# Performance work log

Hardware: AMD Instinct MI355X
Metric: run time of the kernel (lower is better)

## Reference

```python
import jax, jax.numpy as jnp
import numpy as np

# FlowNetC correlation hyperparameters (init_kwargs)
PAD = 4            # pad_size
KERNEL = 1         # kernel_size (1x1 patch)
MD = 4             # max_displacement
STRIDE1 = 1        # stride over output positions
STRIDE2 = 1        # stride over displacements


def setup_inputs() -> dict:
    key = jax.random.key(0)
    k1, k2 = jax.random.split(key)
    input1 = jax.random.normal(k1, (8, 256, 96, 128), dtype=jnp.float32)
    input2 = jax.random.normal(k2, (8, 256, 96, 128), dtype=jnp.float32)
    return {"input1": input1, "input2": input2}


def reference(input1, input2):
    # Cost volume: out[b, d, y, x] = (1/C) * sum_c input1[b,c,y,x] * input2[b,c,y+dy,x+dx]
    # for all displacements (dy, dx) in [-MD, MD] with step STRIDE2.
    # With pad_size == max_displacement, kernel_size == 1, stride1 == 1 the output
    # spatial grid equals the input grid (FlowNetC configuration). Normalization
    # matches correlation_cuda: sumelems = kernel_size^2 * C.
    B, C, H, W = input1.shape
    p2 = jnp.pad(input2, ((0, 0), (0, 0), (PAD, PAD), (PAD, PAD)))
    disp = range(-MD, MD + 1, STRIDE2)  # 9 offsets -> 81 displacement channels
    outs = []
    for dy in disp:
        for dx in disp:
            shifted = jax.lax.dynamic_slice(p2, (0, 0, PAD + dy, PAD + dx), (B, C, H, W))
            # mean over channels == sum / (KERNEL*KERNEL*C) since KERNEL == 1
            outs.append(jnp.mean(input1 * shifted, axis=1))
    return jnp.stack(outs, axis=1)  # [B, 81, H, W]
```

## Files before the change

### kernel.cpp

```cpp
#include <hip/hip_runtime.h>
#include <hip/hip_bf16.h>


#define B_ 8
#define C_ 256
#define H_ 96
#define W_ 128
#define HW_ 12288
#define CHW_ 3145728

#define BUFSZ 40960
#define IN1_OFF 0
#define IN2_OFF 8192
#define IN2_ROWB (32 * 64)

typedef __attribute__((ext_vector_type(8))) short short8;
typedef __attribute__((ext_vector_type(4))) float f32x4;

__device__ __forceinline__ int swz16(int g, int slot) {
    return (g ^ (slot & 3) ^ ((slot >> 2) & 3)) * 16;
}

__global__ __launch_bounds__(512, 2) void corr_mfma5(
    const float* __restrict__ in1,
    const float* __restrict__ in2,
    float* __restrict__ out)
{
    __shared__ __align__(16) char lds[2 * BUFSZ];

    const int tid = threadIdx.x;

    const int blk  = blockIdx.x;
    const int b    = blk & 7;
    const int rest = blk >> 3;
    const int yt   = rest >> 3;
    const int xh   = rest & 7;

    #pragma unroll
    for (int k = 0; k < 10; ++k)
        *(f32x4*)(lds + tid * 16 + k * 8192) = f32x4{0.f, 0.f, 0.f, 0.f};

    const int lane = tid & 63;
    const int wv   = tid >> 6;
    const int ut   = wv & 1;
    const int yrh  = wv >> 1;
    const int ln   = lane & 15;
    const int qd   = lane >> 4;

    const int offA0 = IN1_OFF + ((2 * yrh) * 16 + ln) * 64 + swz16(qd, ln);
    const int pB    = 16 * ut + ln;
    const int offB  = IN2_OFF + ((2 * yrh) * 32 + pB) * 64 + swz16(qd, pB);

    const float* in1b = in1 + (size_t)b * CHW_;
    const float* in2b = in2 + (size_t)b * CHW_;

    const int pp2 = tid & 7;
    const int g2  = (tid >> 3) & 3;
    const int r2i = tid >> 5;
    const int px2 = 4 * pp2;
    const int gx2 = xh * 16 - 8 + px2;
    const int ry2 = yt * 8 - 4 + r2i;
    const bool valid2 = (gx2 >= 0) && (gx2 <= 124) && (ry2 >= 0) && (ry2 < H_);
    const int slot2 = r2i * 32 + px2;
    const float* sp2base = in2b + (size_t)(8 * g2) * HW_ + ry2 * W_ + gx2;

    const int pq1 = tid & 3;
    const int jj1 = (tid >> 2) & 3;
    const int g1  = (tid >> 4) & 3;
    const int r1i = tid >> 6;
    const int px1 = 4 * pq1;
    const int gx1 = xh * 16 + px1;
    const int y1  = yt * 8 + r1i;
    const int slot1 = r1i * 16 + px1;
    const float* sp1base = in1b + (size_t)(8 * g1 + 2 * jj1) * HW_ + y1 * W_ + gx1;

    f32x4 r2[8], r1v[2];

    auto issue = [&](int kc) {
        const size_t ch = (size_t)kc * 32 * HW_;
        if (valid2) {
            #pragma unroll
            for (int j = 0; j < 8; ++j)
                r2[j] = *(const f32x4*)(sp2base + ch + (size_t)j * HW_);
        }
        r1v[0] = *(const f32x4*)(sp1base + ch);
        r1v[1] = *(const f32x4*)(sp1base + ch + HW_);
    };

    auto store = [&](char* __restrict__ buf) {
        if (valid2) {
            #pragma unroll
            for (int p = 0; p < 4; ++p) {
                union { __hip_bfloat162 h2[4]; short8 s8; } u;
                #pragma unroll
                for (int jj = 0; jj < 4; ++jj)
                    u.h2[jj] = __float22bfloat162_rn(float2{r2[2 * jj][p], r2[2 * jj + 1][p]});
                *(short8*)(buf + IN2_OFF + (slot2 + p) * 64 + swz16(g2, slot2 + p)) = u.s8;
            }
        }
        #pragma unroll
        for (int p = 0; p < 4; ++p) {
            __hip_bfloat162 h = __float22bfloat162_rn(float2{r1v[0][p], r1v[1][p]});
            *(__hip_bfloat162*)(buf + IN1_OFF + (slot1 + p) * 64 + swz16(g1, slot1 + p) + 4 * jj1) = h;
        }
    };

    f32x4 acc0[9], acc1[9];
    #pragma unroll
    for (int s = 0; s < 9; ++s) { acc0[s] = f32x4{0.f,0.f,0.f,0.f}; acc1[s] = f32x4{0.f,0.f,0.f,0.f}; }

    __syncthreads();

    issue(0);

    for (int kc = 0; kc < 8; ++kc) {
        char* buf = lds + (kc & 1) * BUFSZ;
        store(buf);
        if (kc < 7) issue(kc + 1);
        asm volatile("s_waitcnt lgkmcnt(0)" ::: "memory");
        __builtin_amdgcn_s_barrier();
        asm volatile("" ::: "memory");
        short8 a0  = *(const short8*)(buf + offA0);
        short8 a1  = *(const short8*)(buf + offA0 + 16 * 64);
        short8 blo = *(const short8*)(buf + offB);
        #pragma unroll
        for (int s = 0; s < 9; ++s) {
            short8 bhi = *(const short8*)(buf + offB + (s + 1) * IN2_ROWB);
            acc0[s] = __builtin_amdgcn_mfma_f32_16x16x32_bf16(a0, blo, acc0[s], 0, 0, 0);
            acc1[s] = __builtin_amdgcn_mfma_f32_16x16x32_bf16(a1, bhi, acc1[s], 0, 0, 0);
            blo = bhi;
        }
    }

    __syncthreads();

    const float scale = 1.0f / 256.0f;
    float* outb = out + (size_t)b * 81 * HW_ + (size_t)(yt * 8) * W_ + xh * 16;

    #pragma unroll
    for (int s = 0; s < 9; ++s) {
        #pragma unroll
        for (int yr = 0; yr < 2; ++yr) {
            const f32x4 a = yr ? acc1[s] : acc0[s];
            const int y = 2 * yrh + yr;
            #pragma unroll
            for (int r = 0; r < 4; ++r) {
                const int m  = qd * 4 + r;
                const int dx = ln - m - 8 + 16 * ut;
                if (dx >= -4 && dx <= 4)
                    *(float*)(lds + ((y * 9 + dx + 4) * 16 + m) * 4) = a[r] * scale;
            }
        }
        asm volatile("s_waitcnt lgkmcnt(0)" ::: "memory");
        __builtin_amdgcn_s_barrier();
        asm volatile("" ::: "memory");
        #pragma unroll
        for (int i = 0; i < 3; ++i) {
            const int pidx = i * 4 + qd;
            if (pidx < 9) {
                const float v = *(const float*)(lds + ((wv * 9 + pidx) * 16 + ln) * 4);
                outb[((size_t)(s * 9 + pidx) * H_ + wv) * W_ + ln] = v;
            }
        }
        asm volatile("s_waitcnt lgkmcnt(0)" ::: "memory");
        __builtin_amdgcn_s_barrier();
        asm volatile("" ::: "memory");
    }
}

extern "C" void kernel_launch(void* const* d_in, const int* in_sizes, int n_in,
                              void* d_out, int out_size, void* d_ws, size_t ws_size,
                              hipStream_t stream) {
    const float* in1 = (const float*)d_in[0];
    const float* in2 = (const float*)d_in[1];
    float* out = (float*)d_out;

    corr_mfma5<<<768, 512, 0, stream>>>(in1, in2, out);
}
```

Before: 247.5 us.

## Pre-convert inputs to swizzled channel-last bf16 workspace and stream via direct LDS loads

Adds a prep kernel that converts both fp32 NCHW inputs into a bf16 channel-blocked, pre-swizzled layout in the workspace. The main kernel then fills LDS with global_load_lds DMA in a two-stage prefetch, with no register staging, conversion or LDS zeroing, and out-of-bounds halo reads point at a zeroed pad. The aim is to cut per-block fp32 reload and conversion overhead for the halo-duplicated input2 tiles and to overlap loads with MFMA. The cost is an extra kernel launch plus a full write and re-read of a bf16 copy of both inputs. A fallback path keeps the old kernel when the workspace is too small.

```diff
diff --git a/kernel.cpp b/kernel.cpp
--- a/kernel.cpp
+++ b/kernel.cpp
@@ -14,6 +14,10 @@
 #define IN2_OFF 8192
 #define IN2_ROWB (32 * 64)
 
+#define PLANEB 786432
+#define IMGWS  50331648
+#define WS_NEED (2ull * IMGWS + 1024ull)
+
 typedef __attribute__((ext_vector_type(8))) short short8;
 typedef __attribute__((ext_vector_type(4))) float f32x4;
 
@@ -21,24 +25,74 @@
     return (g ^ (slot & 3) ^ ((slot >> 2) & 3)) * 16;
 }
 
-__global__ __launch_bounds__(512, 2) void corr_mfma5(
+__device__ __forceinline__ void gload16(const void* g, void* l) {
+    __builtin_amdgcn_global_load_lds(
+        (const __attribute__((address_space(1))) unsigned int*)g,
+        (__attribute__((address_space(3))) unsigned int*)l, 16, 0, 0);
+}
+
+__global__ __launch_bounds__(256) void prep(
     const float* __restrict__ in1,
     const float* __restrict__ in2,
+    char* __restrict__ ws)
+{
+    const int blk = blockIdx.x;
+    const int tid = threadIdx.x;
+
+    if (blk == 0)
+        *(float*)(ws + 2 * (size_t)IMGWS + tid * 4) = 0.f;
+
+    const int img  = (blk >= 768) ? 1 : 0;
+    const int r    = blk - img * 768;
+    const int b    = r & 7;
+    const int rest = r >> 3;
+    const int kc   = rest & 7;
+    const int yo   = rest >> 3;
+
+    const float* src = (img ? in2 : in1) + (size_t)b * CHW_ + (size_t)(kc * 32) * HW_;
+    char* dplane = ws + (size_t)img * IMGWS + (size_t)(b * 8 + kc) * PLANEB;
+
+    const int g  = tid & 3;
+    const int xq = (tid >> 2) & 15;
+    const int yl = tid >> 6;
+
+    #pragma unroll
+    for (int yi = 0; yi < 2; ++yi) {
+        const int y = yo * 8 + yi * 4 + yl;
+        #pragma unroll
+        for (int x2 = 0; x2 < 2; ++x2) {
+            const int px0 = x2 * 64 + xq * 4;
+            f32x4 v[8];
+            #pragma unroll
+            for (int jj = 0; jj < 8; ++jj)
+                v[jj] = *(const f32x4*)(src + (size_t)(8 * g + jj) * HW_ + y * W_ + px0);
+            #pragma unroll
+            for (int j = 0; j < 4; ++j) {
+                const int px = px0 + j;
+                union { __hip_bfloat162 h2[4]; short8 s8; } u;
+                #pragma unroll
+                for (int p = 0; p < 4; ++p)
+                    u.h2[p] = __float22bfloat162_rn(float2{v[2 * p][j], v[2 * p + 1][j]});
+                const int F = img ? ((px & 3) ^ (((px + 8) >> 2) & 3))
+                                  : ((px & 3) ^ ((px >> 2) & 3));
+                *(short8*)(dplane + ((size_t)y * W_ + px) * 64 + (g ^ F) * 16) = u.s8;
+            }
+        }
+    }
+}
+
+__global__ __launch_bounds__(512, 4) void corr_mfma7(
+    const char* __restrict__ ws,
     float* __restrict__ out)
 {
     __shared__ __align__(16) char lds[2 * BUFSZ];
 
     const int tid = threadIdx.x;
-
-    const int blk  = blockIdx.x;
+    const int blk = blockIdx.x;
     const int b    = blk & 7;
     const int rest = blk >> 3;
     const int yt   = rest >> 3;
     const int xh   = rest & 7;
-
-    #pragma unroll
-    for (int k = 0; k < 10; ++k)
-        *(f32x4*)(lds + tid * 16 + k * 8192) = f32x4{0.f, 0.f, 0.f, 0.f};
 
     const int lane = tid & 63;
     const int wv   = tid >> 6;
@@ -51,9 +105,128 @@
     const int pB    = 16 * ut + ln;
     const int offB  = IN2_OFF + ((2 * yrh) * 32 + pB) * 64 + swz16(qd, pB);
 
+    const char* ws1 = ws;
+    const char* ws2 = ws + (size_t)IMGWS;
+    const char* zp  = ws + 2 * (size_t)IMGWS + (lane & 3) * 16;
+    const int b8 = b * 8;
+
+    const int plx   = lane >> 2;
+    const int pos16 = (lane & 3) * 16;
+
+    f32x4 acc0[9], acc1[9];
+    #pragma unroll
+    for (int s = 0; s < 9; ++s) { acc0[s] = f32x4{0.f,0.f,0.f,0.f}; acc1[s] = f32x4{0.f,0.f,0.f,0.f}; }
+
+    auto issue = [&](int kc, char* buf) {
+        const char* p2 = ws2 + (size_t)(b8 + kc) * PLANEB;
+        const char* p1 = ws1 + (size_t)(b8 + kc) * PLANEB;
+        #pragma unroll
+        for (int i = 0; i < 5; ++i) {
+            const int id = wv * 5 + i;
+            if (id < 32) {
+                const int row = id >> 1, seg = id & 1;
+                const int gy = yt * 8 - 4 + row;
+                const int gx = xh * 16 - 8 + seg * 16 + plx;
+                const bool vld = (gy >= 0) && (gy < H_) && (gx >= 0) && (gx < W_);
+                const char* src = vld ? (p2 + (((size_t)gy << 7) + gx) * 64 + pos16) : zp;
+                gload16(src, buf + IN2_OFF + ((row * 32 + seg * 16) << 6));
+            } else {
+                const int row = id - 32;
+                const int gy = yt * 8 + row;
+                const int gx = xh * 16 + plx;
+                const char* src = p1 + (((size_t)gy << 7) + gx) * 64 + pos16;
+                gload16(src, buf + IN1_OFF + (row << 10));
+            }
+        }
+    };
+
+    auto compute = [&](const char* __restrict__ buf) {
+        short8 a0  = *(const short8*)(buf + offA0);
+        short8 a1  = *(const short8*)(buf + offA0 + 16 * 64);
+        short8 blo = *(const short8*)(buf + offB);
+        #pragma unroll
+        for (int s = 0; s < 9; ++s) {
+            short8 bhi = *(const short8*)(buf + offB + (s + 1) * IN2_ROWB);
+            acc0[s] = __builtin_amdgcn_mfma_f32_16x16x32_bf16(a0, blo, acc0[s], 0, 0, 0);
+            acc1[s] = __builtin_amdgcn_mfma_f32_16x16x32_bf16(a1, bhi, acc1[s], 0, 0, 0);
+            blo = bhi;
+        }
+    };
+
+    issue(0, lds);
+    issue(1, lds + BUFSZ);
+
+    #pragma unroll
+    for (int kc = 0; kc < 8; ++kc) {
+        char* buf = lds + (kc & 1) * BUFSZ;
+        if (kc < 7) { asm volatile("s_waitcnt vmcnt(5)" ::: "memory"); }
+        else        { asm volatile("s_waitcnt vmcnt(0)" ::: "memory"); }
+        __builtin_amdgcn_s_barrier();
+        compute(buf);
+        __builtin_amdgcn_s_barrier();
+        if (kc + 2 < 8) issue(kc + 2, buf);
+    }
+
+    const float scale = 1.0f / 256.0f;
+    float* outb = out + (size_t)b * 81 * HW_ + (size_t)(yt * 8) * W_ + xh * 16;
+
+    #pragma unroll
+    for (int s = 0; s < 9; ++s) {
+        #pragma unroll
+        for (int yr = 0; yr < 2; ++yr) {
+            const f32x4 a = yr ? acc1[s] : acc0[s];
+            const int y = 2 * yrh + yr;
+            #pragma unroll
+            for (int r = 0; r < 4; ++r) {
+                const int m  = qd * 4 + r;
+                const int dx = ln - m - 8 + 16 * ut;
+                if (dx >= -4 && dx <= 4)
+                    *(float*)(lds + ((y * 9 + dx + 4) * 16 + m) * 4) = a[r] * scale;
+            }
+        }
+        asm volatile("s_waitcnt lgkmcnt(0)" ::: "memory");
+        __builtin_amdgcn_s_barrier();
+        asm volatile("" ::: "memory");
+        #pragma unroll
+        for (int i = 0; i < 3; ++i) {
+            const int pidx = i * 4 + qd;
+            if (pidx < 9) {
+                const float v = *(const float*)(lds + ((wv * 9 + pidx) * 16 + ln) * 4);
+                outb[((size_t)(s * 9 + pidx) * H_ + wv) * W_ + ln] = v;
+            }
+        }
+        asm volatile("s_waitcnt lgkmcnt(0)" ::: "memory");
+        __builtin_amdgcn_s_barrier();
+        asm volatile("" ::: "memory");
+    }
+}
+
+__global__ __launch_bounds__(512, 2) void corr_fb(
+    const float* __restrict__ in1,
+    const float* __restrict__ in2,
+    float* __restrict__ out)
+{
+    __shared__ __align__(16) char lds[2 * BUFSZ];
+    const int tid = threadIdx.x;
+    const int blk  = blockIdx.x;
+    const int b    = blk & 7;
+    const int rest = blk >> 3;
+    const int yt   = rest >> 3;
+    const int xh   = rest & 7;
+    #pragma unroll
+    for (int k = 0; k < 10; ++k)
+        *(f32x4*)(lds + tid * 16 + k * 8192) = f32x4{0.f, 0.f, 0.f, 0.f};
+    const int lane = tid & 63;
+    const int wv   = tid >> 6;
+    const int ut   = wv & 1;
+    const int yrh  = wv >> 1;
+    const int ln   = lane & 15;
+    const int qd   = lane >> 4;
+    const int offA0 = IN1_OFF + ((2 * yrh) * 16 + ln) * 64 + swz16(qd, ln);
+    const int pB    = 16 * ut + ln;
+    const int offB  = IN2_OFF + ((2 * yrh) * 32 + pB) * 64 + swz16(qd, pB);
     const float* in1b = in1 + (size_t)b * CHW_;
     const float* in2b = in2 + (size_t)b * CHW_;
-
     const int pp2 = tid & 7;
     const int g2  = (tid >> 3) & 3;
     const int r2i = tid >> 5;
@@ -63,7 +236,6 @@
     const bool valid2 = (gx2 >= 0) && (gx2 <= 124) && (ry2 >= 0) && (ry2 < H_);
     const int slot2 = r2i * 32 + px2;
     const float* sp2base = in2b + (size_t)(8 * g2) * HW_ + ry2 * W_ + gx2;
-
     const int pq1 = tid & 3;
     const int jj1 = (tid >> 2) & 3;
     const int g1  = (tid >> 4) & 3;
@@ -73,9 +245,7 @@
     const int y1  = yt * 8 + r1i;
     const int slot1 = r1i * 16 + px1;
     const float* sp1base = in1b + (size_t)(8 * g1 + 2 * jj1) * HW_ + y1 * W_ + gx1;
-
     f32x4 r2[8], r1v[2];
-
     auto issue = [&](int kc) {
         const size_t ch = (size_t)kc * 32 * HW_;
         if (valid2) {
@@ -86,7 +256,6 @@
         r1v[0] = *(const f32x4*)(sp1base + ch);
         r1v[1] = *(const f32x4*)(sp1base + ch + HW_);
     };
-
     auto store = [&](char* __restrict__ buf) {
         if (valid2) {
             #pragma unroll
@@ -104,15 +273,11 @@
             *(__hip_bfloat162*)(buf + IN1_OFF + (slot1 + p) * 64 + swz16(g1, slot1 + p) + 4 * jj1) = h;
         }
     };
-
     f32x4 acc0[9], acc1[9];
     #pragma unroll
     for (int s = 0; s < 9; ++s) { acc0[s] = f32x4{0.f,0.f,0.f,0.f}; acc1[s] = f32x4{0.f,0.f,0.f,0.f}; }
-
     __syncthreads();
-
     issue(0);
-
     for (int kc = 0; kc < 8; ++kc) {
         char* buf = lds + (kc & 1) * BUFSZ;
         store(buf);
@@ -131,12 +296,9 @@
             blo = bhi;
         }
     }
-
     __syncthreads();
-
     const float scale = 1.0f / 256.0f;
     float* outb = out + (size_t)b * 81 * HW_ + (size_t)(yt * 8) * W_ + xh * 16;
-
     #pragma unroll
     for (int s = 0; s < 9; ++s) {
         #pragma unroll
@@ -175,5 +337,10 @@
     const float* in2 = (const float*)d_in[1];
     float* out = (float*)d_out;
 
-    corr_mfma5<<<768, 512, 0, stream>>>(in1, in2, out);
-}
+    if (ws_size >= WS_NEED && d_ws != nullptr) {
+        prep<<<1536, 256, 0, stream>>>(in1, in2, (char*)d_ws);
+        corr_mfma7<<<768, 512, 0, stream>>>((const char*)d_ws, out);
+    } else {
+        corr_fb<<<768, 512, 0, stream>>>(in1, in2, out);
+    }
+}
```

Measured after the change: 317.2 us. 1.28x slower.
